# Kernel tuning notes

Hardware: AMD Instinct MI355X
Metric: run time of the kernel (lower is better)

Reference implementation:

```python
import jax, jax.numpy as jnp
import numpy as np

N = 250000      # total nodes = B * NN
E = 4000000     # edges (avg degree 16)
NODE = 4        # node_size
EDGE = 1        # edge_size
HID = 32        # hidden_dim
NN = 50         # nnodes per graph
NF = 3          # num_factories


def setup_inputs() -> dict:
    key = jax.random.key(0)
    ks = jax.random.split(key, 10)
    def glorot(k, shp, fan_in):
        return (jax.random.normal(k, shp, jnp.float32) / np.sqrt(fan_in)).astype(jnp.float32)
    x = jax.random.normal(ks[0], (N, NODE), jnp.float32)
    edge_index = jax.random.randint(ks[1], (2, E), 0, N, dtype=jnp.int64)
    edge_attr = jax.random.normal(ks[2], (E, EDGE), jnp.float32)
    high = jnp.ones((NF,), jnp.float32)
    D_in = 2 * NODE + EDGE
    D_cat = NODE + HID
    W1 = glorot(ks[3], (D_in, HID), D_in); b1 = jnp.zeros((HID,), jnp.float32)
    W2 = glorot(ks[4], (HID, HID), HID);   b2 = jnp.zeros((HID,), jnp.float32)
    Wc = glorot(ks[5], (D_cat, 1), D_cat);  bc = jnp.zeros((1,), jnp.float32)
    Wmu = glorot(ks[6], (D_cat, 1), D_cat); bmu = jnp.zeros((1,), jnp.float32)
    Wsig = glorot(ks[7], (D_cat, 1), D_cat); bsig = jnp.zeros((1,), jnp.float32)
    return dict(x=x, edge_index=edge_index, edge_attr=edge_attr, high=high,
                W1=W1, b1=b1, W2=W2, b2=b2, Wc=Wc, bc=bc,
                Wmu=Wmu, bmu=bmu, Wsig=Wsig, bsig=bsig)


def reference(x, edge_index, edge_attr, high, W1, b1, W2, b2, Wc, bc, Wmu, bmu, Wsig, bsig):
    # EdgeConv (flow='target_to_source', aggr='add'): x_i = x[row], x_j = x[col], scatter-add at row
    row, col = edge_index[0], edge_index[1]
    msg_in = jnp.concatenate([x[row], x[col], edge_attr], axis=1)      # [E, 2*NODE+EDGE]
    msg = jax.nn.relu(msg_in @ W1 + b1) @ W2 + b2                      # [E, HID]
    agg = jax.ops.segment_sum(msg, row, num_segments=x.shape[0])       # [N, HID]
    x_pp = jnp.concatenate([x, agg], axis=1).reshape(-1, NN, NODE + HID)  # [B, NN, D_cat]
    tail = x_pp[:, -NF:]                                               # [B, NF, D_cat]
    alpha = jax.nn.softplus((tail @ Wmu + bmu).squeeze(-1) + 1e-20) + 1e-20   # [B, NF]
    beta = jax.nn.softplus((tail @ Wsig + bsig).squeeze(-1) + 1e-20) + 1e-20  # [B, NF]
    conc = jax.nn.softplus((x_pp @ Wc + bc).squeeze(-1) + 1e-10)       # [B, NN]
    inventory_act = conc / (conc.sum() + 1e-20)                        # deterministic Dirichlet mean-style
    order_act = alpha / (alpha + beta) * high                          # deterministic Beta mean * high
    return jnp.concatenate([inventory_act, order_act], axis=1)         # [B, NN+NF]
```

## Files before the change

### kernel.cpp

```cpp
#include <hip/hip_runtime.h>

#define N_NODES 250000
#define N_EDGES 4000000
#define HID 32
#define NN 50
#define NF 3
#define OUT_COLS (NN + NF)

#define NB 512
#define NBKT ((N_NODES + NB - 1) / NB)
#define PCHUNK 4096
#define NPBLK ((N_EDGES + PCHUNK - 1) / PCHUNK)
#define BCAP_SLOT 8832

typedef float float2v __attribute__((ext_vector_type(2)));

__device__ __forceinline__ float softplus_f(float v) {
    return fmaxf(v, 0.0f) + log1pf(expf(-fabsf(v)));
}

__device__ __forceinline__ float2v pk_fma(float a, float2v b, float2v c) {
    float2v av = {a, a};
    return __builtin_elementwise_fma(av, b, c);
}

__global__ __launch_bounds__(1024, 8) void part_kernel(
    const int* __restrict__ ei, const float* __restrict__ ea,
    int* __restrict__ gcursor, int2* __restrict__ bpay)
{
    __shared__ int2 srec[PCHUNK];
    __shared__ int hist[NBKT];
    __shared__ int excl[NBKT];
    __shared__ int gbase[NBKT];
    __shared__ unsigned char bkt[PCHUNK];
    __shared__ int wsum[16];

    int t = threadIdx.x;
    int lane = t & 63, wid = t >> 6;
    int cbb = blockIdx.x * PCHUNK;
    int cnt = N_EDGES - cbb; if (cnt > PCHUNK) cnt = PCHUNK;

    for (int i = t; i < NBKT; i += 1024) hist[i] = 0;
    __syncthreads();

    int e0 = cbb + t * 4;
    int r[4], rk[4];
    bool full = (e0 + 4 <= N_EDGES);
    if (full) {
        int4 ra = *(const int4*)(ei + e0);
        r[0] = ra.x; r[1] = ra.y; r[2] = ra.z; r[3] = ra.w;
    } else {
        #pragma unroll
        for (int j = 0; j < 4; j++) r[j] = (e0 + j < N_EDGES) ? ei[e0 + j] : 0;
    }
    #pragma unroll
    for (int j = 0; j < 4; j++)
        rk[j] = (e0 + j < N_EDGES) ? atomicAdd(&hist[r[j] >> 9], 1) : 0;
    __syncthreads();

    int hv = (t < NBKT) ? hist[t] : 0;
    int v = hv;
    #pragma unroll
    for (int off = 1; off < 64; off <<= 1) {
        int u = __shfl_up(v, off, 64);
        if (lane >= off) v += u;
    }
    if (lane == 63) wsum[wid] = v;
    __syncthreads();
    if (wid == 0) {
        int w = (lane < 16) ? wsum[lane] : 0;
        #pragma unroll
        for (int off = 1; off < 16; off <<= 1) {
            int u = __shfl_up(w, off, 64);
            if (lane >= off) w += u;
        }
        if (lane < 16) wsum[lane] = w;
    }
    __syncthreads();
    int wbase = (wid > 0) ? wsum[wid - 1] : 0;
    int myExcl = wbase + (v - hv);
    if (t < NBKT) {
        excl[t] = myExcl;
        int base = 0;
        if (hv > 0) base = atomicAdd(&gcursor[t], hv);
        gbase[t] = t * BCAP_SLOT + base;
    }
    __syncthreads();

    if (full) {
        int4 ca = *(const int4*)(ei + N_EDGES + e0);
        float4 aa = *(const float4*)(ea + e0);
        int c[4] = {ca.x, ca.y, ca.z, ca.w};
        float a[4] = {aa.x, aa.y, aa.z, aa.w};
        #pragma unroll
        for (int j = 0; j < 4; j++) {
            int bb = r[j] >> 9;
            int lrow = r[j] & (NB - 1);
            int slot = excl[bb] + rk[j];
            srec[slot] = make_int2(c[j] | (lrow << 18), __float_as_int(a[j]));
            bkt[slot] = (unsigned char)(bb & 0xFF);
        }
    } else {
        #pragma unroll
        for (int j = 0; j < 4; j++) {
            if (e0 + j < N_EDGES) {
                int bb = r[j] >> 9;
                int lrow = r[j] & (NB - 1);
                int col  = ei[N_EDGES + e0 + j];
                float at = ea[e0 + j];
                int slot = excl[bb] + rk[j];
                srec[slot] = make_int2(col | (lrow << 18), __float_as_int(at));
                bkt[slot] = (unsigned char)(bb & 0xFF);
            }
        }
    }
    __syncthreads();

    for (int s = t; s < cnt; s += 1024) {
        int2 rec = srec[s];
        int c1 = bkt[s];
        int c2 = c1 + 256;
        int bb = (c2 < NBKT && excl[c2] <= s) ? c2 : c1;
        int gpos = gbase[bb] + (s - excl[bb]);
        if (gpos < (bb + 1) * BCAP_SLOT)
            bpay[gpos] = rec;
    }
}

__global__ __launch_bounds__(512, 4) void bucket_kernel(
    const int2* __restrict__ bpay, const int* __restrict__ gcursor,
    const float* __restrict__ x,
    const float* __restrict__ W1, const float* __restrict__ b1,
    const float* __restrict__ W2, const float* __restrict__ b2,
    const float* __restrict__ Wc, const float* __restrict__ bc,
    const float* __restrict__ Wmu, const float* __restrict__ bmu,
    const float* __restrict__ Wsig, const float* __restrict__ bsig,
    const float* __restrict__ high,
    float* __restrict__ sum_out, float* __restrict__ out)
{
    __shared__ int2 srec[BCAP_SLOT];
    __shared__ int hist[NB];
    __shared__ int nbeg[NB];
    __shared__ int perm[NB];
    __shared__ int dhist[64];
    __shared__ int wsum[8];
    __shared__ float bsum[8];
    __shared__ float fW[3][32];
    __shared__ float fB[3];

    int b = blockIdx.x;
    int t = threadIdx.x;
    int lane = t & 63, wid = t >> 6;
    int beg = b * BCAP_SLOT;
    int cnt = gcursor[b]; if (cnt > BCAP_SLOT) cnt = BCAP_SLOT;

    hist[t] = 0;
    if (t < 96) {
        int vsel = t >> 5;
        int k = t & 31;
        const float* Wv = (vsel == 0) ? Wc : (vsel == 1) ? Wmu : Wsig;
        float f = 0.0f;
        #pragma unroll
        for (int j = 0; j < 32; j++) f = fmaf(W2[k * 32 + j], Wv[4 + j], f);
        fW[vsel][k] = f;
    } else if (t < 99) {
        int vsel = t - 96;
        const float* Wv = (vsel == 0) ? Wc : (vsel == 1) ? Wmu : Wsig;
        float f = 0.0f;
        #pragma unroll
        for (int j = 0; j < 32; j++) f = fmaf(b2[j], Wv[4 + j], f);
        fB[vsel] = f;
    }
    __syncthreads();

    int2 rec[18];
    int rk[18];
    #pragma unroll
    for (int k = 0; k < 9; k++) {
        int s = (k * 512 + t) * 2;
        int4 pp = *(const int4*)(bpay + beg + s);
        rec[2 * k]     = make_int2(pp.x, pp.y);
        rec[2 * k + 1] = make_int2(pp.z, pp.w);
        rk[2 * k]     = (s < cnt)     ? atomicAdd(&hist[(pp.x >> 18) & (NB - 1)], 1) : 0;
        rk[2 * k + 1] = (s + 1 < cnt) ? atomicAdd(&hist[(pp.z >> 18) & (NB - 1)], 1) : 0;
    }
    __syncthreads();

    int hv = hist[t];
    int v = hv;
    #pragma unroll
    for (int off = 1; off < 64; off <<= 1) {
        int u = __shfl_up(v, off, 64);
        if (lane >= off) v += u;
    }
    if (lane == 63) wsum[wid] = v;
    __syncthreads();
    if (wid == 0) {
        int w = (lane < 8) ? wsum[lane] : 0;
        #pragma unroll
        for (int off = 1; off < 8; off <<= 1) {
            int u = __shfl_up(w, off, 64);
            if (lane >= off) w += u;
        }
        if (lane < 8) wsum[lane] = w;
    }
    __syncthreads();
    int wbase = (wid > 0) ? wsum[wid - 1] : 0;
    nbeg[t] = wbase + (v - hv);
    __syncthreads();

    #pragma unroll
    for (int k = 0; k < 9; k++) {
        int s = (k * 512 + t) * 2;
        if (s < cnt) {
            int lrow = (rec[2 * k].x >> 18) & (NB - 1);
            srec[nbeg[lrow] + rk[2 * k]] = rec[2 * k];
        }
        if (s + 1 < cnt) {
            int lrow = (rec[2 * k + 1].x >> 18) & (NB - 1);
            srec[nbeg[lrow] + rk[2 * k + 1]] = rec[2 * k + 1];
        }
    }

    int bin = min(hv, 63);
    if (t < 64) dhist[t] = 0;
    __syncthreads();
    atomicAdd(&dhist[bin], 1);
    __syncthreads();
    if (wid == 0) {
        int dv = dhist[lane];
        int sv = dv;
        #pragma unroll
        for (int off = 1; off < 64; off <<= 1) {
            int u = __shfl_up(sv, off, 64);
            if (lane >= off) sv += u;
        }
        dhist[lane] = sv - dv;
    }
    __syncthreads();
    int pos = atomicAdd(&dhist[bin], 1);
    perm[pos] = t;
    __syncthreads();

    int tt = perm[t];
    int n = b * NB + tt;
    bool valid = (n < N_NODES);
    int nn = valid ? n : 0;
    int deg = valid ? hist[tt] : 0;
    int s0 = nbeg[tt];

    float4 xr = *(const float4*)(x + 4 * (size_t)nn);

    const float2v* W1v = (const float2v*)W1;
    const float2v* b1v = (const float2v*)b1;

    float2v arow[16];
    #pragma unroll
    for (int k2 = 0; k2 < 16; k2++) {
        float2v a = b1v[k2];
        a = pk_fma(xr.x, W1v[0 * 16 + k2], a);
        a = pk_fma(xr.y, W1v[1 * 16 + k2], a);
        a = pk_fma(xr.z, W1v[2 * 16 + k2], a);
        a = pk_fma(xr.w, W1v[3 * 16 + k2], a);
        arow[k2] = a;
    }

    float2v acc2[16];
    #pragma unroll
    for (int j2 = 0; j2 < 16; j2++) { float2v z = {0.f, 0.f}; acc2[j2] = z; }

    float mk0[4], ev0[4];
    float4 xc0[4];
    #pragma unroll
    for (int j = 0; j < 4; j++) {
        bool ok = j < deg;
        int idx = ok ? (s0 + j) : 0;
        int2 rr = srec[idx];
        mk0[j] = ok ? 1.0f : 0.0f;
        int col = ok ? (rr.x & 0x3FFFF) : 0;
        ev0[j] = ok ? __int_as_float(rr.y) : 0.0f;
        xc0[j] = *(const float4*)(x + 4 * (size_t)col);
    }

    for (int c = 0; c < deg; c += 4) {
        int c1 = c + 4;
        float mk1[4], ev1[4];
        float4 xc1[4];
        #pragma unroll
        for (int j = 0; j < 4; j++) {
            bool ok = (c1 + j) < deg;
            int idx = ok ? (s0 + c1 + j) : 0;
            int2 rr = srec[idx];
            mk1[j] = ok ? 1.0f : 0.0f;
            int col = ok ? (rr.x & 0x3FFFF) : 0;
            ev1[j] = ok ? __int_as_float(rr.y) : 0.0f;
            xc1[j] = *(const float4*)(x + 4 * (size_t)col);
        }

        #pragma unroll
        for (int k2 = 0; k2 < 16; k2++) {
            float2v w4 = W1v[4 * 16 + k2];
            float2v w5 = W1v[5 * 16 + k2];
            float2v w6 = W1v[6 * 16 + k2];
            float2v w7 = W1v[7 * 16 + k2];
            float2v w8 = W1v[8 * 16 + k2];
            #pragma unroll
            for (int j = 0; j < 4; j++) {
                float2v a = arow[k2];
                a = pk_fma(xc0[j].x, w4, a);
                a = pk_fma(xc0[j].y, w5, a);
                a = pk_fma(xc0[j].z, w6, a);
                a = pk_fma(xc0[j].w, w7, a);
                a = pk_fma(ev0[j],   w8, a);
                float2v zero = {0.0f, 0.0f};
                a = __builtin_elementwise_max(a, zero);
                float2v mm = {mk0[j], mk0[j]};
                acc2[k2] = __builtin_elementwise_fma(a, mm, acc2[k2]);
            }
        }

        #pragma unroll
        for (int j = 0; j < 4; j++) {
            mk0[j] = mk1[j]; ev0[j] = ev1[j]; xc0[j] = xc1[j];
        }
    }

    float c_val = 0.0f;
    if (valid) {
        float* accf = (float*)acc2;
        float fdeg = (float)deg;

        float zc = fmaf(fdeg, fB[0], bc[0]);
        zc = fmaf(xr.x, Wc[0], zc);
        zc = fmaf(xr.y, Wc[1], zc);
        zc = fmaf(xr.z, Wc[2], zc);
        zc = fmaf(xr.w, Wc[3], zc);
        #pragma unroll
        for (int j = 0; j < 32; j++) zc = fmaf(accf[j], fW[0][j], zc);
        c_val = softplus_f(zc + 1e-10f);

        int g = n / NN;
        int i = n - g * NN;
        out[(size_t)g * OUT_COLS + i] = c_val;

        if (i >= NN - NF) {
            float zm = fmaf(fdeg, fB[1], bmu[0]);
            float zs = fmaf(fdeg, fB[2], bsig[0]);
            zm = fmaf(xr.x, Wmu[0], zm);   zs = fmaf(xr.x, Wsig[0], zs);
            zm = fmaf(xr.y, Wmu[1], zm);   zs = fmaf(xr.y, Wsig[1], zs);
            zm = fmaf(xr.z, Wmu[2], zm);   zs = fmaf(xr.z, Wsig[2], zs);
            zm = fmaf(xr.w, Wmu[3], zm);   zs = fmaf(xr.w, Wsig[3], zs);
            #pragma unroll
            for (int j = 0; j < 32; j++) {
                zm = fmaf(accf[j], fW[1][j], zm);
                zs = fmaf(accf[j], fW[2][j], zs);
            }
            float alpha = softplus_f(zm + 1e-20f) + 1e-20f;
            float beta  = softplus_f(zs + 1e-20f) + 1e-20f;
            int k = i - (NN - NF);
            out[(size_t)g * OUT_COLS + NN + k] = alpha / (alpha + beta) * high[k];
        }
    }

    float s = c_val;
    #pragma unroll
    for (int off = 32; off > 0; off >>= 1) s += __shfl_down(s, off, 64);
    if (lane == 0) bsum[wid] = s;
    __syncthreads();
    if (t == 0) {
        float tt2 = 0.0f;
        #pragma unroll
        for (int j = 0; j < 8; j++) tt2 += bsum[j];
        atomicAdd(sum_out, tt2);
    }
}

__global__ __launch_bounds__(256) void div_kernel(
    const float* __restrict__ sum_in, float* __restrict__ out)
{
    int n = blockIdx.x * 256 + threadIdx.x;
    if (n >= N_NODES) return;
    float inv = 1.0f / (*sum_in + 1e-20f);
    int g = n / NN;
    int i = n - g * NN;
    out[(size_t)g * OUT_COLS + i] *= inv;
}

extern "C" void kernel_launch(void* const* d_in, const int* in_sizes, int n_in,
                              void* d_out, int out_size, void* d_ws, size_t ws_size,
                              hipStream_t stream)
{
    const float* x    = (const float*)d_in[0];
    const int*   ei   = (const int*)d_in[1];
    const float* ea   = (const float*)d_in[2];
    const float* high = (const float*)d_in[3];
    const float* W1   = (const float*)d_in[4];
    const float* b1   = (const float*)d_in[5];
    const float* W2   = (const float*)d_in[6];
    const float* b2   = (const float*)d_in[7];
    const float* Wc   = (const float*)d_in[8];
    const float* bc   = (const float*)d_in[9];
    const float* Wmu  = (const float*)d_in[10];
    const float* bmu  = (const float*)d_in[11];
    const float* Wsig = (const float*)d_in[12];
    const float* bsig = (const float*)d_in[13];
    float* out = (float*)d_out;

    char* ws = (char*)d_ws;
    int2*  bpay    = (int2*)ws;
    int*   gcursor = (int*)(ws + 34550784);
    float* ssum    = (float*)(ws + 34552832);

    hipMemsetAsync(gcursor, 0, 2052, stream);

    part_kernel<<<NPBLK, 1024, 0, stream>>>(ei, ea, gcursor, bpay);
    bucket_kernel<<<NBKT, 512, 0, stream>>>(
        bpay, gcursor, x, W1, b1, W2, b2, Wc, bc, Wmu, bmu, Wsig, bsig,
        high, ssum, out);
    div_kernel<<<(N_NODES + 255) / 256, 256, 0, stream>>>(ssum, out);
}
```

Before: 185.7 us.

## Split each node's edge loop across two threads with LDS partial-sum reduction

The bucket kernel grows from 512 to 1024 threads per block. Each node's edge range is split between a pair of threads, and the two 32-wide accumulators are combined through shared memory, reusing the record buffer, before the output head is computed. The aim is to shorten the per-thread serial edge loop and raise the number of waves in flight, since only about two blocks land per CU. In exchange it adds extra barriers and an LDS reduction. The launch bound of 1024 threads with 8 waves per EU tightens the register budget and could cause spills of the accumulator arrays. The record-load loop also now reads past the bucket's slot capacity.

```diff
diff --git a/kernel.cpp b/kernel.cpp
--- a/kernel.cpp
+++ b/kernel.cpp
@@ -127,7 +127,7 @@
     }
 }
 
-__global__ __launch_bounds__(512, 4) void bucket_kernel(
+__global__ __launch_bounds__(1024, 8) void bucket_kernel(
     const int2* __restrict__ bpay, const int* __restrict__ gcursor,
     const float* __restrict__ x,
     const float* __restrict__ W1, const float* __restrict__ b1,
@@ -143,8 +143,8 @@
     __shared__ int nbeg[NB];
     __shared__ int perm[NB];
     __shared__ int dhist[64];
-    __shared__ int wsum[8];
-    __shared__ float bsum[8];
+    __shared__ int wsum[16];
+    __shared__ float bsum[16];
     __shared__ float fW[3][32];
     __shared__ float fB[3];
 
@@ -154,17 +154,17 @@
     int beg = b * BCAP_SLOT;
     int cnt = gcursor[b]; if (cnt > BCAP_SLOT) cnt = BCAP_SLOT;
 
-    hist[t] = 0;
-    if (t < 96) {
-        int vsel = t >> 5;
+    if (t < NB) hist[t] = 0;
+    if (t >= 512 && t < 608) {
+        int vsel = (t - 512) >> 5;
         int k = t & 31;
         const float* Wv = (vsel == 0) ? Wc : (vsel == 1) ? Wmu : Wsig;
         float f = 0.0f;
         #pragma unroll
         for (int j = 0; j < 32; j++) f = fmaf(W2[k * 32 + j], Wv[4 + j], f);
         fW[vsel][k] = f;
-    } else if (t < 99) {
-        int vsel = t - 96;
+    } else if (t >= 608 && t < 611) {
+        int vsel = t - 608;
         const float* Wv = (vsel == 0) ? Wc : (vsel == 1) ? Wmu : Wsig;
         float f = 0.0f;
         #pragma unroll
@@ -173,11 +173,11 @@
     }
     __syncthreads();
 
-    int2 rec[18];
-    int rk[18];
-    #pragma unroll
-    for (int k = 0; k < 9; k++) {
-        int s = (k * 512 + t) * 2;
+    int2 rec[10];
+    int rk[10];
+    #pragma unroll
+    for (int k = 0; k < 5; k++) {
+        int s = (k * 1024 + t) * 2;
         int4 pp = *(const int4*)(bpay + beg + s);
         rec[2 * k]     = make_int2(pp.x, pp.y);
         rec[2 * k + 1] = make_int2(pp.z, pp.w);
@@ -186,14 +186,14 @@
     }
     __syncthreads();
 
-    int hv = hist[t];
+    int hv = (t < NB) ? hist[t] : 0;
     int v = hv;
     #pragma unroll
     for (int off = 1; off < 64; off <<= 1) {
         int u = __shfl_up(v, off, 64);
         if (lane >= off) v += u;
     }
-    if (lane == 63) wsum[wid] = v;
+    if (lane == 63 && wid < 8) wsum[wid] = v;
     __syncthreads();
     if (wid == 0) {
         int w = (lane < 8) ? wsum[lane] : 0;
@@ -205,13 +205,15 @@
         if (lane < 8) wsum[lane] = w;
     }
     __syncthreads();
-    int wbase = (wid > 0) ? wsum[wid - 1] : 0;
-    nbeg[t] = wbase + (v - hv);
-    __syncthreads();
-
-    #pragma unroll
-    for (int k = 0; k < 9; k++) {
-        int s = (k * 512 + t) * 2;
+    if (t < NB) {
+        int wbase = (wid > 0) ? wsum[wid - 1] : 0;
+        nbeg[t] = wbase + (v - hv);
+    }
+    __syncthreads();
+
+    #pragma unroll
+    for (int k = 0; k < 5; k++) {
+        int s = (k * 1024 + t) * 2;
         if (s < cnt) {
             int lrow = (rec[2 * k].x >> 18) & (NB - 1);
             srec[nbeg[lrow] + rk[2 * k]] = rec[2 * k];
@@ -222,10 +224,10 @@
         }
     }
 
+    if (t < 64) dhist[t] = 0;
+    __syncthreads();
     int bin = min(hv, 63);
-    if (t < 64) dhist[t] = 0;
-    __syncthreads();
-    atomicAdd(&dhist[bin], 1);
+    if (t < NB) atomicAdd(&dhist[bin], 1);
     __syncthreads();
     if (wid == 0) {
         int dv = dhist[lane];
@@ -238,16 +240,22 @@
         dhist[lane] = sv - dv;
     }
     __syncthreads();
-    int pos = atomicAdd(&dhist[bin], 1);
-    perm[pos] = t;
-    __syncthreads();
-
-    int tt = perm[t];
-    int n = b * NB + tt;
+    if (t < NB) {
+        int pos = atomicAdd(&dhist[bin], 1);
+        perm[pos] = t;
+    }
+    __syncthreads();
+
+    int pr = t >> 1;
+    int slice = t & 1;
+    int node = perm[pr];
+    int n = b * NB + node;
     bool valid = (n < N_NODES);
     int nn = valid ? n : 0;
-    int deg = valid ? hist[tt] : 0;
-    int s0 = nbeg[tt];
+    int deg = valid ? hist[node] : 0;
+    int half = (deg + 1) >> 1;
+    int myCnt = slice ? (deg - half) : half;
+    int s0 = nbeg[node] + slice * half;
 
     float4 xr = *(const float4*)(x + 4 * (size_t)nn);
 
@@ -273,7 +281,7 @@
     float4 xc0[4];
     #pragma unroll
     for (int j = 0; j < 4; j++) {
-        bool ok = j < deg;
+        bool ok = j < myCnt;
         int idx = ok ? (s0 + j) : 0;
         int2 rr = srec[idx];
         mk0[j] = ok ? 1.0f : 0.0f;
@@ -282,13 +290,13 @@
         xc0[j] = *(const float4*)(x + 4 * (size_t)col);
     }
 
-    for (int c = 0; c < deg; c += 4) {
+    for (int c = 0; c < myCnt; c += 4) {
         int c1 = c + 4;
         float mk1[4], ev1[4];
         float4 xc1[4];
         #pragma unroll
         for (int j = 0; j < 4; j++) {
-            bool ok = (c1 + j) < deg;
+            bool ok = (c1 + j) < myCnt;
             int idx = ok ? (s0 + c1 + j) : 0;
             int2 rr = srec[idx];
             mk1[j] = ok ? 1.0f : 0.0f;
@@ -325,9 +333,27 @@
         }
     }
 
+    __syncthreads();
+    float* fbuf = (float*)srec;
+    float* accf = (float*)acc2;
+    if (slice == 1) {
+        #pragma unroll
+        for (int k = 0; k < 32; k++) {
+            int kk = (k + lane) & 31;
+            fbuf[node * 32 + kk] = accf[kk];
+        }
+    }
+    __syncthreads();
+    if (slice == 0) {
+        #pragma unroll
+        for (int k = 0; k < 32; k++) {
+            int kk = (k + lane) & 31;
+            accf[kk] += fbuf[node * 32 + kk];
+        }
+    }
+
     float c_val = 0.0f;
-    if (valid) {
-        float* accf = (float*)acc2;
+    if (valid && slice == 0) {
         float fdeg = (float)deg;
 
         float zc = fmaf(fdeg, fB[0], bc[0]);
@@ -370,7 +396,7 @@
     if (t == 0) {
         float tt2 = 0.0f;
         #pragma unroll
-        for (int j = 0; j < 8; j++) tt2 += bsum[j];
+        for (int j = 0; j < 16; j++) tt2 += bsum[j];
         atomicAdd(sum_out, tt2);
     }
 }
@@ -414,7 +440,7 @@
     hipMemsetAsync(gcursor, 0, 2052, stream);
 
     part_kernel<<<NPBLK, 1024, 0, stream>>>(ei, ea, gcursor, bpay);
-    bucket_kernel<<<NBKT, 512, 0, stream>>>(
+    bucket_kernel<<<NBKT, 1024, 0, stream>>>(
         bpay, gcursor, x, W1, b1, W2, b2, Wc, bc, Wmu, bmu, Wsig, bsig,
         high, ssum, out);
     div_kernel<<<(N_NODES + 255) / 256, 256, 0, stream>>>(ssum, out);
```

Result: slower. 492.1 us (+165.0%).
